# Optimization experiments

Measured on AMD Instinct MI355X. Metric: run time of the kernel, lower is better.

The kernel has to match this reference:

```python
import jax, jax.numpy as jnp
import numpy as np

NUM_HEADS = 12


def get_rel_pos(q_size, k_size, rel_pos):
    # rel_pos: (2*max(q,k)-1, head_dim); sizes match table here so no resize.
    max_rel_dist = int(2 * max(q_size, k_size) - 1)
    if rel_pos.shape[0] != max_rel_dist:
        rel_pos = jax.image.resize(rel_pos, (max_rel_dist, rel_pos.shape[1]), method='linear')
    q_coords = jnp.arange(q_size)[:, None] * max(k_size / q_size, 1.0)
    k_coords = jnp.arange(k_size)[None, :] * max(q_size / k_size, 1.0)
    rel = (q_coords - k_coords + (k_size - 1) * max(q_size / k_size, 1.0)).astype(jnp.int32)
    return rel_pos[rel.reshape(-1)].reshape(q_size, k_size, -1)  # (q, k, head_dim)


def setup_inputs() -> dict:
    key = jax.random.key(0)
    ks = jax.random.split(key, 7)
    B, H, W, C = 8, 32, 32, 768
    head_dim = C // NUM_HEADS
    return {
        'x': jax.random.normal(ks[0], (B, H, W, C), jnp.float32),
        'w_qkv': jax.random.normal(ks[1], (C, 3 * C), jnp.float32) * 0.02,
        'b_qkv': jnp.zeros((3 * C,), jnp.float32),
        'rel_pos_h': jax.random.normal(ks[2], (2 * H - 1, head_dim), jnp.float32) * 0.02,
        'rel_pos_w': jax.random.normal(ks[3], (2 * W - 1, head_dim), jnp.float32) * 0.02,
        'w_proj': jax.random.normal(ks[4], (C, C), jnp.float32) * 0.02,
        'b_proj': jnp.zeros((C,), jnp.float32),
    }


def reference(x, w_qkv, b_qkv, rel_pos_h, rel_pos_w, w_proj, b_proj):
    B, H, W, C = x.shape
    heads = NUM_HEADS
    hd = C // heads
    S = H * W
    qkv = x @ w_qkv + b_qkv                                  # (B,H,W,3C)
    qkv = qkv.reshape(B, S, 3, heads, hd).transpose(2, 0, 3, 1, 4)
    qkv = qkv.reshape(3, B * heads, S, hd)
    q, k, v = qkv[0], qkv[1], qkv[2]
    attn = (q * hd ** -0.5) @ k.transpose(0, 2, 1)           # (B*heads, S, S)
    rh = get_rel_pos(H, H, rel_pos_h)                        # (H,H,hd)
    rw = get_rel_pos(W, W, rel_pos_w)                        # (W,W,hd)
    r_q = q.reshape(B * heads, H, W, hd)
    rel_h = jnp.einsum('bhwc,hkc->bhwk', r_q, rh)
    rel_w = jnp.einsum('bhwc,wkc->bhwk', r_q, rw)
    attn = (attn.reshape(B * heads, H, W, H, W)
            + rel_h[:, :, :, :, None]
            + rel_w[:, :, :, None, :]).reshape(B * heads, S, S)
    attn = jax.nn.softmax(attn, axis=-1)
    out = (attn @ v).reshape(B, heads, H, W, hd).transpose(0, 2, 3, 1, 4).reshape(B, H, W, C)
    return out @ w_proj + b_proj
```

## Files before the change

### kernel.cpp

```cpp
#include <hip/hip_runtime.h>
#include <hip/hip_bf16.h>

#define BATCH 8
#define SEQ   1024
#define CH    768
#define NH    12
#define HD    64
#define BH    96
#define N_QKV 2304

#define LOG2E 1.44269504088896f

typedef __attribute__((ext_vector_type(8))) short bfrag;
typedef __attribute__((ext_vector_type(4))) short short4v;
typedef __attribute__((ext_vector_type(4))) float ffrag;

__device__ __forceinline__ short f2bf(float x) {
    __hip_bfloat16 h = __float2bfloat16(x);
    return *reinterpret_cast<short*>(&h);
}
__device__ __forceinline__ float bf2f(short b) {
    __hip_bfloat16 h;
    *reinterpret_cast<short*>(&h) = b;
    return __bfloat162float(h);
}
__device__ __forceinline__ void split2(float x, short& hi, short& lo) {
    short h = f2bf(x);
    hi = h;
    lo = f2bf(x - bf2f(h));
}
__device__ __forceinline__ void async_copy16(void* lds, const void* g) {
    __builtin_amdgcn_global_load_lds(
        (const __attribute__((address_space(1))) void*)g,
        (__attribute__((address_space(3))) void*)lds, 16, 0, 0);
}

__global__ __launch_bounds__(256) void prep(
    const float* __restrict__ x,
    const float* __restrict__ w_qkv, const float* __restrict__ w_proj,
    short* __restrict__ Xh,
    short* __restrict__ WqhT,
    short* __restrict__ WphT, short* __restrict__ WplT)
{
    __shared__ float ts[32][33];
    const int tid = threadIdx.x;
    const int bid = blockIdx.x;

    if (bid < 512) {
        const int n4 = (BATCH * SEQ * CH) / 4;
        for (int i = bid * 256 + tid; i < n4; i += 512 * 256) {
            float4 f = ((const float4*)x)[i];
            short4v h;
            h[0] = f2bf(f.x); h[1] = f2bf(f.y); h[2] = f2bf(f.z); h[3] = f2bf(f.w);
            ((short4v*)Xh)[i] = h;
        }
        return;
    }
    if (bid < 2240) {
        int t = bid - 512;
        const int bx = t % 72, by = t / 72;
        const int r0 = by * 32, c0 = bx * 32;
        #pragma unroll
        for (int i = 0; i < 4; ++i) {
            int idx = tid + i * 256;
            int rr = idx >> 5, cc = idx & 31;
            ts[rr][cc] = w_qkv[(size_t)(r0 + rr) * N_QKV + c0 + cc];
        }
        __syncthreads();
        #pragma unroll
        for (int i = 0; i < 4; ++i) {
            int idx = tid + i * 256;
            int rr = idx >> 5, cc = idx & 31;
            WqhT[(size_t)(c0 + rr) * CH + r0 + cc] = f2bf(ts[cc][rr]);
        }
        return;
    }
    {
        int t = bid - 2240;
        const int bx = t % 24, by = t / 24;
        const int r0 = by * 32, c0 = bx * 32;
        #pragma unroll
        for (int i = 0; i < 4; ++i) {
            int idx = tid + i * 256;
            int rr = idx >> 5, cc = idx & 31;
            ts[rr][cc] = w_proj[(size_t)(r0 + rr) * CH + c0 + cc];
        }
        __syncthreads();
        #pragma unroll
        for (int i = 0; i < 4; ++i) {
            int idx = tid + i * 256;
            int rr = idx >> 5, cc = idx & 31;
            short h, l;
            split2(ts[cc][rr], h, l);
            WphT[(size_t)(c0 + rr) * CH + r0 + cc] = h;
            WplT[(size_t)(c0 + rr) * CH + r0 + cc] = l;
        }
    }
}

__device__ __forceinline__ void gemm_core1(
    short* lds,
    const short* __restrict__ Ah, const short* __restrict__ BhT,
    int m0, int n0, ffrag acc[4][4])
{
    const int tid = threadIdx.x;
    const int wave = tid >> 6, lane = tid & 63;
    const int quad = lane >> 4, l16 = lane & 15;
    const int wm = (wave & 1) * 64, wn = (wave >> 1) * 64;

    const int arr  = wave >> 1;
    const int half = wave & 1;
    const short* src = arr ? BhT : Ah;
    const int row0 = (arr ? n0 : m0) + half * 64;
    const size_t lane_off = (size_t)(lane >> 3) * CH + (size_t)((lane & 7) ^ (lane >> 3)) * 8;
    const short* sbase = src + (size_t)row0 * CH + lane_off;
    short* ldsw = lds + arr * 8192 + half * 4096;

    for (int c = 0; c < 12; ++c) {
        __syncthreads();
        #pragma unroll
        for (int i = 0; i < 8; ++i)
            async_copy16(ldsw + i * 512, sbase + (size_t)i * 8 * CH + c * 64);
        __syncthreads();

        #pragma unroll
        for (int kc = 0; kc < 2; ++kc) {
            bfrag ah[4], bh[4];
            const int xs = ((kc * 4 + quad) ^ (l16 & 7)) * 8;
            #pragma unroll
            for (int i = 0; i < 4; ++i) {
                ah[i] = *(const bfrag*)&lds[(wm + i * 16 + l16) * 64 + xs];
                bh[i] = *(const bfrag*)&lds[8192 + (wn + i * 16 + l16) * 64 + xs];
            }
            #pragma unroll
            for (int mi = 0; mi < 4; ++mi)
                #pragma unroll
                for (int ni = 0; ni < 4; ++ni)
                    acc[mi][ni] = __builtin_amdgcn_mfma_f32_16x16x32_bf16(ah[mi], bh[ni], acc[mi][ni], 0, 0, 0);
        }
    }
}

__device__ __forceinline__ void gemm_core3(
    short* lds,
    const short* __restrict__ Ah, const short* __restrict__ Al,
    const short* __restrict__ BhT, const short* __restrict__ BlT,
    int m0, int n0, ffrag acc[4][4])
{
    const int tid = threadIdx.x;
    const int wave = tid >> 6, lane = tid & 63;
    const int quad = lane >> 4, l16 = lane & 15;
    const int wm = (wave & 1) * 64, wn = (wave >> 1) * 64;

    const short* src;
    int row0;
    if (wave == 0)      { src = Ah;  row0 = m0; }
    else if (wave == 1) { src = Al;  row0 = m0; }
    else if (wave == 2) { src = BhT; row0 = n0; }
    else                { src = BlT; row0 = n0; }
    const size_t lane_off = (size_t)(lane >> 3) * CH + (size_t)((lane & 7) ^ (lane >> 3)) * 8;
    const short* sbase = src + (size_t)row0 * CH + lane_off;
    short* ldsw = lds + wave * 8192;

    for (int c = 0; c < 12; ++c) {
        __syncthreads();
        #pragma unroll
        for (int i = 0; i < 16; ++i)
            async_copy16(ldsw + i * 512, sbase + (size_t)i * 8 * CH + c * 64);
        __syncthreads();

        #pragma unroll
        for (int kc = 0; kc < 2; ++kc) {
            bfrag ah[4], al[4], bh[4], bl[4];
            const int xs = ((kc * 4 + quad) ^ (l16 & 7)) * 8;
            #pragma unroll
            for (int i = 0; i < 4; ++i) {
                int ra = (wm + i * 16 + l16) * 64 + xs;
                int rb = (wn + i * 16 + l16) * 64 + xs;
                ah[i] = *(const bfrag*)&lds[ra];
                al[i] = *(const bfrag*)&lds[8192 + ra];
                bh[i] = *(const bfrag*)&lds[16384 + rb];
                bl[i] = *(const bfrag*)&lds[24576 + rb];
            }
            #pragma unroll
            for (int mi = 0; mi < 4; ++mi)
                #pragma unroll
                for (int ni = 0; ni < 4; ++ni) {
                    acc[mi][ni] = __builtin_amdgcn_mfma_f32_16x16x32_bf16(ah[mi], bh[ni], acc[mi][ni], 0, 0, 0);
                    acc[mi][ni] = __builtin_amdgcn_mfma_f32_16x16x32_bf16(ah[mi], bl[ni], acc[mi][ni], 0, 0, 0);
                    acc[mi][ni] = __builtin_amdgcn_mfma_f32_16x16x32_bf16(al[mi], bh[ni], acc[mi][ni], 0, 0, 0);
                }
        }
    }
}

__global__ __launch_bounds__(256) void gemm_qkv_mfma(
    const short* __restrict__ Xh,
    const short* __restrict__ WhT,
    const float* __restrict__ bias,
    short* __restrict__ qh, short* __restrict__ kh, short* __restrict__ vT)
{
    __shared__ short lds[2 * 8192];
    const int id  = blockIdx.x;
    const int xcd = id & 7;
    const int per = id >> 3;
    const int mi_ = per / 9, ni_ = per % 9;
    const int m0 = ((xcd & 3) * 16 + mi_) * 128;
    const int n0 = ((xcd >> 2) * 9 + ni_) * 128;
    const int which = n0 / CH;

    ffrag acc[4][4];
    #pragma unroll
    for (int i = 0; i < 4; ++i)
        #pragma unroll
        for (int j = 0; j < 4; ++j) acc[i][j] = (ffrag){0.f, 0.f, 0.f, 0.f};

    gemm_core1(lds, Xh, WhT, m0, n0, acc);

    const int tid = threadIdx.x;
    const int wave = tid >> 6, lane = tid & 63;
    const int quad = lane >> 4, l16 = lane & 15;
    const int wm = (wave & 1) * 64, wn = (wave >> 1) * 64;
    const int b = m0 >> 10;

    #pragma unroll
    for (int ni = 0; ni < 4; ++ni) {
        int n = n0 + wn + ni * 16 + l16;
        float bv = bias[n];
        int nin = n - which * CH;
        int head = nin >> 6, d = nin & 63;
        #pragma unroll
        for (int mi = 0; mi < 4; ++mi) {
            if (which == 2) {
                int s_base = (m0 & 1023) + wm + mi * 16 + quad * 4;
                short4v pk;
                #pragma unroll
                for (int r = 0; r < 4; ++r) pk[r] = f2bf(acc[mi][ni][r] + bv);
                *(short4v*)&vT[((size_t)(b * NH + head) * HD + d) * SEQ + s_base] = pk;
            } else {
                const float scale = (which == 0) ? 0.125f * LOG2E : 1.0f;
                short* dst = (which == 0) ? qh : kh;
                #pragma unroll
                for (int r = 0; r < 4; ++r) {
                    int m = m0 + wm + mi * 16 + quad * 4 + r;
                    int s = m & 1023;
                    dst[((size_t)(b * NH + head) * SEQ + s) * HD + d] =
                        f2bf((acc[mi][ni][r] + bv) * scale);
                }
            }
        }
    }
}

__global__ __launch_bounds__(256) void gemm_proj_mfma(
    const short* __restrict__ Ah, const short* __restrict__ Al,
    const short* __restrict__ WhT, const short* __restrict__ WlT,
    const float* __restrict__ bias, float* __restrict__ out)
{
    __shared__ short lds[4 * 8192];
    const int id  = blockIdx.x;
    const int xcd = id & 7;
    const int per = id >> 3;
    const int m0 = (xcd * 8 + per / 6) * 128;
    const int n0 = (per % 6) * 128;

    ffrag acc[4][4];
    #pragma unroll
    for (int i = 0; i < 4; ++i)
        #pragma unroll
        for (int j = 0; j < 4; ++j) acc[i][j] = (ffrag){0.f, 0.f, 0.f, 0.f};

    gemm_core3(lds, Ah, Al, WhT, WlT, m0, n0, acc);

    const int tid = threadIdx.x;
    const int wave = tid >> 6, lane = tid & 63;
    const int quad = lane >> 4, l16 = lane & 15;
    const int wm = (wave & 1) * 64, wn = (wave >> 1) * 64;

    #pragma unroll
    for (int ni = 0; ni < 4; ++ni) {
        int n = n0 + wn + ni * 16 + l16;
        float bv = bias[n];
        #pragma unroll
        for (int mi = 0; mi < 4; ++mi)
            #pragma unroll
            for (int r = 0; r < 4; ++r) {
                int m = m0 + wm + mi * 16 + quad * 4 + r;
                out[(size_t)m * CH + n] = acc[mi][ni][r] + bv;
            }
    }
}

__global__ __launch_bounds__(256, 3) void attn_kernel(
    const short* __restrict__ qh,
    const short* __restrict__ kh_g, const short* __restrict__ vT_g,
    const float* __restrict__ rph,
    const float* __restrict__ rpw,
    short* __restrict__ aoh, short* __restrict__ aol)
{
    const int fid   = blockIdx.x;
    const int xcd   = fid & 7;
    const int inner = fid >> 3;
    const int s0    = (inner & 7) * 128;
    const int bh    = xcd * 12 + (inner >> 3);

    const int tid  = threadIdx.x;
    const int wave = tid >> 6;
    const int lane = tid & 63;
    const int quad = lane >> 4;
    const int l16  = lane & 15;

    __shared__ short Kh[64 * 64];
    __shared__ short Vth[64 * 64];
    __shared__ short Th[128][68];
    __shared__ short Tw_Ps[128 * 68];

    bfrag qfh[2][2];
    #pragma unroll
    for (int g = 0; g < 2; ++g) {
        const size_t qrow = ((size_t)bh * SEQ + s0 + wave * 32 + g * 16 + l16) * HD;
        #pragma unroll
        for (int kc = 0; kc < 2; ++kc)
            qfh[g][kc] = *(const bfrag*)(qh + qrow + kc * 32 + quad * 8);
    }

    #pragma unroll
    for (int table = 0; table < 2; ++table) {
        const float* tbl = table ? rpw : rph;
        #pragma unroll
        for (int n0r = 0; n0r < 64; n0r += 16) {
            int r = n0r + l16;
            bfrag bfr[2];
            #pragma unroll
            for (int kc = 0; kc < 2; ++kc) {
                if (r < 63) {
                    const float* trow = tbl + (size_t)r * HD + kc * 32 + quad * 8;
                    float4 f0 = *(const float4*)(trow);
                    float4 f1 = *(const float4*)(trow + 4);
                    float xs[8] = {f0.x, f0.y, f0.z, f0.w, f1.x, f1.y, f1.z, f1.w};
                    #pragma unroll
                    for (int j = 0; j < 8; ++j) bfr[kc][j] = f2bf(xs[j]);
                } else {
                    #pragma unroll
                    for (int j = 0; j < 8; ++j) bfr[kc][j] = 0;
                }
            }
            #pragma unroll
            for (int g = 0; g < 2; ++g) {
                ffrag acc = {0.f, 0.f, 0.f, 0.f};
                acc = __builtin_amdgcn_mfma_f32_16x16x32_bf16(qfh[g][0], bfr[0], acc, 0, 0, 0);
                acc = __builtin_amdgcn_mfma_f32_16x16x32_bf16(qfh[g][1], bfr[1], acc, 0, 0, 0);
                int row = wave * 32 + g * 16 + quad * 4;
                #pragma unroll
                for (int reg = 0; reg < 4; ++reg) {
                    short v = f2bf(acc[reg] * 8.0f);
                    if (table) Tw_Ps[(row + reg) * 68 + n0r + l16] = v;
                    else       Th[row + reg][n0r + l16] = v;
                }
            }
        }
    }

    float tw_r[2][2][4];
    #pragma unroll
    for (int g = 0; g < 2; ++g) {
        int qloc = wave * 32 + g * 16 + l16;
        int wq = g * 16 + l16;
        #pragma unroll
        for (int p = 0; p < 2; ++p)
            #pragma unroll
            for (int reg = 0; reg < 4; ++reg)
                tw_r[g][p][reg] = bf2f(Tw_Ps[qloc * 68 + (wq - (p * 16 + quad * 4 + reg) + 31)]);
    }
    const int hq_w = (s0 >> 5) + wave;

    float l_part[2] = {0.f, 0.f};
    ffrag Ot[2][4];
    #pragma unroll
    for (int g = 0; g < 2; ++g)
        #pragma unroll
        for (int t = 0; t < 4; ++t) Ot[g][t] = (ffrag){0.f, 0.f, 0.f, 0.f};

    const size_t bh_koff = (size_t)bh * SEQ * HD;
    const size_t bh_voff = (size_t)bh * HD * SEQ;
    const size_t klane = (size_t)(lane >> 3) * HD + (size_t)((lane & 7) ^ (lane >> 3)) * 8;
    const size_t vlane = (size_t)(lane >> 3) * SEQ + (size_t)((lane & 7) ^ (lane >> 3)) * 8;

    for (int c = 0; c < 16; ++c) {
        __syncthreads();
        #pragma unroll
        for (int j = 0; j < 2; ++j) {
            int i = wave * 2 + j;
            async_copy16(Kh + i * 512,
                         kh_g + bh_koff + (size_t)(c * 64 + i * 8) * HD + klane);
            async_copy16(Vth + i * 512,
                         vT_g + bh_voff + (size_t)(i * 8) * SEQ + c * 64 + vlane);
        }
        __syncthreads();

        float th_r[2][2];
        #pragma unroll
        for (int g = 0; g < 2; ++g) {
            int qloc = wave * 32 + g * 16 + l16;
            th_r[g][0] = bf2f(Th[qloc][hq_w - 2 * c + 31]);
            th_r[g][1] = bf2f(Th[qloc][hq_w - 2 * c - 1 + 31]);
        }

        #pragma unroll
        for (int kt = 0; kt < 4; ++kt) {
            bfrag kbh[2];
            #pragma unroll
            for (int kc = 0; kc < 2; ++kc) {
                int xs = ((kc * 4 + quad) ^ (l16 & 7)) * 8;
                kbh[kc] = *(const bfrag*)&Kh[(kt * 16 + l16) * 64 + xs];
            }
            const int hp = kt >> 1, wp = kt & 1;
            #pragma unroll
            for (int g = 0; g < 2; ++g) {
                ffrag acc;
                #pragma unroll
                for (int reg = 0; reg < 4; ++reg)
                    acc[reg] = th_r[g][hp] + tw_r[g][wp][reg];
                acc = __builtin_amdgcn_mfma_f32_16x16x32_bf16(kbh[0], qfh[g][0], acc, 0, 0, 0);
                acc = __builtin_amdgcn_mfma_f32_16x16x32_bf16(kbh[1], qfh[g][1], acc, 0, 0, 0);
                short4v pk;
                #pragma unroll
                for (int reg = 0; reg < 4; ++reg) {
                    float p = exp2f(acc[reg]);
                    l_part[g] += p;
                    pk[reg] = f2bf(p);
                }
                *(short4v*)&Tw_Ps[(wave * 32 + g * 16 + l16) * 68 + kt * 16 + quad * 4] = pk;
            }
        }

        bfrag pf[2][2];
        #pragma unroll
        for (int g = 0; g < 2; ++g)
            #pragma unroll
            for (int kc2 = 0; kc2 < 2; ++kc2) {
                int base = (wave * 32 + g * 16 + l16) * 68 + kc2 * 32 + quad * 8;
                short4v lo = *(const short4v*)&Tw_Ps[base];
                short4v hi = *(const short4v*)&Tw_Ps[base + 4];
                bfrag p;
                #pragma unroll
                for (int j = 0; j < 4; ++j) { p[j] = lo[j]; p[j + 4] = hi[j]; }
                pf[g][kc2] = p;
            }

        #pragma unroll
        for (int t = 0; t < 4; ++t) {
            int d = t * 16 + l16;
            int x0 = ((0 + quad) ^ (l16 & 7)) * 8;
            int x1 = ((4 + quad) ^ (l16 & 7)) * 8;
            bfrag vh0 = *(const bfrag*)&Vth[d * 64 + x0];
            bfrag vh1 = *(const bfrag*)&Vth[d * 64 + x1];
            #pragma unroll
            for (int g = 0; g < 2; ++g) {
                Ot[g][t] = __builtin_amdgcn_mfma_f32_16x16x32_bf16(pf[g][0], vh0, Ot[g][t], 0, 0, 0);
                Ot[g][t] = __builtin_amdgcn_mfma_f32_16x16x32_bf16(pf[g][1], vh1, Ot[g][t], 0, 0, 0);
            }
        }
    }

    {
        int b = bh / NH, head = bh % NH;
        #pragma unroll
        for (int g = 0; g < 2; ++g) {
            float r = l_part[g];
            r += __shfl_xor(r, 16, 64);
            r += __shfl_xor(r, 32, 64);
            float invl = 1.f / r;
            float inv[4];
            #pragma unroll
            for (int reg = 0; reg < 4; ++reg)
                inv[reg] = __shfl(invl, quad * 4 + reg, 16);
            #pragma unroll
            for (int t = 0; t < 4; ++t) {
                #pragma unroll
                for (int reg = 0; reg < 4; ++reg) {
                    int s_ = s0 + wave * 32 + g * 16 + quad * 4 + reg;
                    int d = t * 16 + l16;
                    size_t idx = ((size_t)(b * SEQ + s_)) * CH + head * HD + d;
                    short h, l;
                    split2(Ot[g][t][reg] * inv[reg], h, l);
                    aoh[idx] = h;
                    aol[idx] = l;
                }
            }
        }
    }
}

extern "C" void kernel_launch(void* const* d_in, const int* in_sizes, int n_in,
                              void* d_out, int out_size, void* d_ws, size_t ws_size,
                              hipStream_t stream) {
    const float* x       = (const float*)d_in[0];
    const float* w_qkv   = (const float*)d_in[1];
    const float* b_qkv   = (const float*)d_in[2];
    const float* rph     = (const float*)d_in[3];
    const float* rpw     = (const float*)d_in[4];
    const float* w_proj  = (const float*)d_in[5];
    const float* b_proj  = (const float*)d_in[6];
    float* out = (float*)d_out;

    const size_t NTOK = (size_t)BATCH * SEQ;
    const size_t XSZ  = NTOK * CH;
    const size_t WQSZ = (size_t)N_QKV * CH;
    const size_t WPSZ = (size_t)CH * CH;
    short* Xh   = (short*)d_ws;
    short* AoL  = Xh + XSZ;
    short* WqhT = AoL + XSZ;
    short* WphT = WqhT + WQSZ;
    short* WplT = WphT + WPSZ;
    short* qh = WplT + WPSZ;
    short* kh = qh + XSZ;
    short* vT = kh + XSZ;
    short* aoh = Xh;
    short* aol = AoL;

    prep<<<dim3(2816), 256, 0, stream>>>(x, w_qkv, w_proj,
                                         Xh, WqhT, WphT, WplT);
    gemm_qkv_mfma<<<dim3(1152), 256, 0, stream>>>(Xh, WqhT, b_qkv,
                                                  qh, kh, vT);
    attn_kernel<<<dim3(768), 256, 0, stream>>>(qh, kh, vT,
                                               rph, rpw, aoh, aol);
    gemm_proj_mfma<<<dim3(384), 256, 0, stream>>>(aoh, aol, WphT, WplT,
                                                  b_proj, out);
}
```

Measured before the change: 224.5 us.

## Register-prefetch next K/V chunk and raise wave priority around MFMAs

Replaces the per-chunk async global-to-LDS copies with register double-buffering: the next chunk's K and V^T tiles are loaded into registers while the current chunk is computed, then written to LDS after the barrier. The loop is unrolled by two with a lambda so the A/B register sets swap without copies. It also wraps the MFMA sequences in s_setprio to favour matrix issue across waves. The cost is extra VGPRs, which may reduce occupancy, and LDS stores now go through registers instead of direct async copies.

Result: no change. 220.9 us (-1.6%).

```diff
diff --git a/kernel.cpp b/kernel.cpp
--- a/kernel.cpp
+++ b/kernel.cpp
@@ -315,6 +315,23 @@
     __shared__ short Th[128][68];
     __shared__ short Tw_Ps[128 * 68];
 
+    const size_t bh_koff = (size_t)bh * SEQ * HD;
+    const size_t bh_voff = (size_t)bh * HD * SEQ;
+    const size_t klane = (size_t)(lane >> 3) * HD + (size_t)((lane & 7) ^ (lane >> 3)) * 8;
+    const size_t vlane = (size_t)(lane >> 3) * SEQ + (size_t)((lane & 7) ^ (lane >> 3)) * 8;
+
+    const short* kbase = kh_g + bh_koff + klane;
+    const short* vbase = vT_g + bh_voff + vlane;
+    const int i0 = wave * 2;
+    short* KhW0 = Kh  + i0 * 512 + lane * 8;
+    short* VtW0 = Vth + i0 * 512 + lane * 8;
+
+    int4 kA0, kA1, vA0, vA1, kB0, kB1, vB0, vB1;
+    kA0 = *(const int4*)(kbase + (size_t)(i0 * 8) * HD);
+    kA1 = *(const int4*)(kbase + (size_t)(i0 * 8 + 8) * HD);
+    vA0 = *(const int4*)(vbase + (size_t)(i0 * 8) * SEQ);
+    vA1 = *(const int4*)(vbase + (size_t)(i0 * 8 + 8) * SEQ);
+
     bfrag qfh[2][2];
     #pragma unroll
     for (int g = 0; g < 2; ++g) {
@@ -381,21 +398,21 @@
         #pragma unroll
         for (int t = 0; t < 4; ++t) Ot[g][t] = (ffrag){0.f, 0.f, 0.f, 0.f};
 
-    const size_t bh_koff = (size_t)bh * SEQ * HD;
-    const size_t bh_voff = (size_t)bh * HD * SEQ;
-    const size_t klane = (size_t)(lane >> 3) * HD + (size_t)((lane & 7) ^ (lane >> 3)) * 8;
-    const size_t vlane = (size_t)(lane >> 3) * SEQ + (size_t)((lane & 7) ^ (lane >> 3)) * 8;
-
-    for (int c = 0; c < 16; ++c) {
-        __syncthreads();
-        #pragma unroll
-        for (int j = 0; j < 2; ++j) {
-            int i = wave * 2 + j;
-            async_copy16(Kh + i * 512,
-                         kh_g + bh_koff + (size_t)(c * 64 + i * 8) * HD + klane);
-            async_copy16(Vth + i * 512,
-                         vT_g + bh_voff + (size_t)(i * 8) * SEQ + c * 64 + vlane);
-        }
+    auto chunk = [&](int c, const int4& ck0, const int4& ck1,
+                     const int4& cv0, const int4& cv1,
+                     int4& nk0, int4& nk1, int4& nv0, int4& nv1) {
+        __syncthreads();
+        if (c < 15) {
+            const int cn = c + 1;
+            nk0 = *(const int4*)(kbase + (size_t)(cn * 64 + i0 * 8) * HD);
+            nk1 = *(const int4*)(kbase + (size_t)(cn * 64 + i0 * 8 + 8) * HD);
+            nv0 = *(const int4*)(vbase + (size_t)(i0 * 8) * SEQ + cn * 64);
+            nv1 = *(const int4*)(vbase + (size_t)(i0 * 8 + 8) * SEQ + cn * 64);
+        }
+        *(int4*)KhW0         = ck0;
+        *(int4*)(KhW0 + 512) = ck1;
+        *(int4*)VtW0         = cv0;
+        *(int4*)(VtW0 + 512) = cv1;
         __syncthreads();
 
         float th_r[2][2];
@@ -421,8 +438,10 @@
                 #pragma unroll
                 for (int reg = 0; reg < 4; ++reg)
                     acc[reg] = th_r[g][hp] + tw_r[g][wp][reg];
+                __builtin_amdgcn_s_setprio(1);
                 acc = __builtin_amdgcn_mfma_f32_16x16x32_bf16(kbh[0], qfh[g][0], acc, 0, 0, 0);
                 acc = __builtin_amdgcn_mfma_f32_16x16x32_bf16(kbh[1], qfh[g][1], acc, 0, 0, 0);
+                __builtin_amdgcn_s_setprio(0);
                 short4v pk;
                 #pragma unroll
                 for (int reg = 0; reg < 4; ++reg) {
@@ -455,12 +474,19 @@
             int x1 = ((4 + quad) ^ (l16 & 7)) * 8;
             bfrag vh0 = *(const bfrag*)&Vth[d * 64 + x0];
             bfrag vh1 = *(const bfrag*)&Vth[d * 64 + x1];
+            __builtin_amdgcn_s_setprio(1);
             #pragma unroll
             for (int g = 0; g < 2; ++g) {
                 Ot[g][t] = __builtin_amdgcn_mfma_f32_16x16x32_bf16(pf[g][0], vh0, Ot[g][t], 0, 0, 0);
                 Ot[g][t] = __builtin_amdgcn_mfma_f32_16x16x32_bf16(pf[g][1], vh1, Ot[g][t], 0, 0, 0);
             }
-        }
+            __builtin_amdgcn_s_setprio(0);
+        }
+    };
+
+    for (int cc = 0; cc < 8; ++cc) {
+        chunk(2 * cc,     kA0, kA1, vA0, vA1, kB0, kB1, vB0, vB1);
+        chunk(2 * cc + 1, kB0, kB1, vB0, vB1, kA0, kA1, vA0, vA1);
     }
 
     {
```

## Double-buffer K in LDS with register prefetch and load V fragments directly

Applied to the files above, without the earlier changes.

Replaces the per-chunk async copy of K and V^T into LDS, which was bracketed by two barriers, with a register-staged double-buffered K tile. The next chunk's K is prefetched into registers two chunks ahead, and each loop iteration now needs only one barrier. V fragments are loaded straight from global memory into registers instead of going through LDS, and the MFMA sections are wrapped with s_setprio. The aim is to hide global-memory latency and cut sync overhead, at the cost of more VGPRs, which may lower occupancy. Direct V loads also lose any LDS reuse.

Measured after the change: 223.2 us. About the same (-0.6%).

```diff
diff --git a/kernel.cpp b/kernel.cpp
--- a/kernel.cpp
+++ b/kernel.cpp
@@ -310,10 +310,32 @@
     const int quad = lane >> 4;
     const int l16  = lane & 15;
 
-    __shared__ short Kh[64 * 64];
-    __shared__ short Vth[64 * 64];
+    __shared__ short Kb[2][64 * 64];
     __shared__ short Th[128][68];
     __shared__ short Tw_Ps[128 * 68];
+
+    const size_t bh_koff = (size_t)bh * SEQ * HD;
+    const size_t bh_voff = (size_t)bh * HD * SEQ;
+    const size_t klane = (size_t)(lane >> 3) * HD + (size_t)((lane & 7) ^ (lane >> 3)) * 8;
+
+    const short* kbase = kh_g + bh_koff + klane;
+    const int i0 = wave * 2;
+    const int kw_off = i0 * 512 + lane * 8;
+
+    const short* vfbase = vT_g + bh_voff + (size_t)l16 * SEQ + quad * 8;
+
+    int4 kA0, kA1;
+    int4 kw0, kw1;
+    int4 vf[4][2];
+    kA0 = *(const int4*)(kbase + (size_t)(i0 * 8) * HD);
+    kA1 = *(const int4*)(kbase + (size_t)(i0 * 8 + 8) * HD);
+    #pragma unroll
+    for (int t = 0; t < 4; ++t)
+        #pragma unroll
+        for (int kc2 = 0; kc2 < 2; ++kc2)
+            vf[t][kc2] = *(const int4*)(vfbase + (size_t)(t * 16) * SEQ + kc2 * 32);
+    kw0 = *(const int4*)(kbase + (size_t)(64 + i0 * 8) * HD);
+    kw1 = *(const int4*)(kbase + (size_t)(64 + i0 * 8 + 8) * HD);
 
     bfrag qfh[2][2];
     #pragma unroll
@@ -374,6 +396,10 @@
     }
     const int hq_w = (s0 >> 5) + wave;
 
+    *(int4*)&Kb[0][kw_off]       = kA0;
+    *(int4*)&Kb[0][kw_off + 512] = kA1;
+    __syncthreads();
+
     float l_part[2] = {0.f, 0.f};
     ffrag Ot[2][4];
     #pragma unroll
@@ -381,22 +407,18 @@
         #pragma unroll
         for (int t = 0; t < 4; ++t) Ot[g][t] = (ffrag){0.f, 0.f, 0.f, 0.f};
 
-    const size_t bh_koff = (size_t)bh * SEQ * HD;
-    const size_t bh_voff = (size_t)bh * HD * SEQ;
-    const size_t klane = (size_t)(lane >> 3) * HD + (size_t)((lane & 7) ^ (lane >> 3)) * 8;
-    const size_t vlane = (size_t)(lane >> 3) * SEQ + (size_t)((lane & 7) ^ (lane >> 3)) * 8;
-
     for (int c = 0; c < 16; ++c) {
-        __syncthreads();
-        #pragma unroll
-        for (int j = 0; j < 2; ++j) {
-            int i = wave * 2 + j;
-            async_copy16(Kh + i * 512,
-                         kh_g + bh_koff + (size_t)(c * 64 + i * 8) * HD + klane);
-            async_copy16(Vth + i * 512,
-                         vT_g + bh_voff + (size_t)(i * 8) * SEQ + c * 64 + vlane);
-        }
-        __syncthreads();
+        short* Kw       = &Kb[(c + 1) & 1][0];
+        const short* Kr = &Kb[c & 1][0];
+
+        if (c < 15) {
+            *(int4*)&Kw[kw_off]       = kw0;
+            *(int4*)&Kw[kw_off + 512] = kw1;
+        }
+        if (c < 14) {
+            kw0 = *(const int4*)(kbase + (size_t)((c + 2) * 64 + i0 * 8) * HD);
+            kw1 = *(const int4*)(kbase + (size_t)((c + 2) * 64 + i0 * 8 + 8) * HD);
+        }
 
         float th_r[2][2];
         #pragma unroll
@@ -412,7 +434,7 @@
             #pragma unroll
             for (int kc = 0; kc < 2; ++kc) {
                 int xs = ((kc * 4 + quad) ^ (l16 & 7)) * 8;
-                kbh[kc] = *(const bfrag*)&Kh[(kt * 16 + l16) * 64 + xs];
+                kbh[kc] = *(const bfrag*)&Kr[(kt * 16 + l16) * 64 + xs];
             }
             const int hp = kt >> 1, wp = kt & 1;
             #pragma unroll
@@ -421,8 +443,10 @@
                 #pragma unroll
                 for (int reg = 0; reg < 4; ++reg)
                     acc[reg] = th_r[g][hp] + tw_r[g][wp][reg];
+                __builtin_amdgcn_s_setprio(1);
                 acc = __builtin_amdgcn_mfma_f32_16x16x32_bf16(kbh[0], qfh[g][0], acc, 0, 0, 0);
                 acc = __builtin_amdgcn_mfma_f32_16x16x32_bf16(kbh[1], qfh[g][1], acc, 0, 0, 0);
+                __builtin_amdgcn_s_setprio(0);
                 short4v pk;
                 #pragma unroll
                 for (int reg = 0; reg < 4; ++reg) {
@@ -450,17 +474,27 @@
 
         #pragma unroll
         for (int t = 0; t < 4; ++t) {
-            int d = t * 16 + l16;
-            int x0 = ((0 + quad) ^ (l16 & 7)) * 8;
-            int x1 = ((4 + quad) ^ (l16 & 7)) * 8;
-            bfrag vh0 = *(const bfrag*)&Vth[d * 64 + x0];
-            bfrag vh1 = *(const bfrag*)&Vth[d * 64 + x1];
+            bfrag vh0 = *reinterpret_cast<const bfrag*>(&vf[t][0]);
+            bfrag vh1 = *reinterpret_cast<const bfrag*>(&vf[t][1]);
+            __builtin_amdgcn_s_setprio(1);
             #pragma unroll
             for (int g = 0; g < 2; ++g) {
                 Ot[g][t] = __builtin_amdgcn_mfma_f32_16x16x32_bf16(pf[g][0], vh0, Ot[g][t], 0, 0, 0);
                 Ot[g][t] = __builtin_amdgcn_mfma_f32_16x16x32_bf16(pf[g][1], vh1, Ot[g][t], 0, 0, 0);
             }
-        }
+            __builtin_amdgcn_s_setprio(0);
+        }
+
+        if (c < 15) {
+            #pragma unroll
+            for (int t = 0; t < 4; ++t)
+                #pragma unroll
+                for (int kc2 = 0; kc2 < 2; ++kc2)
+                    vf[t][kc2] = *(const int4*)(vfbase + (size_t)(t * 16) * SEQ
+                                                + (c + 1) * 64 + kc2 * 32);
+        }
+
+        __syncthreads();
     }
 
     {
```
